# Kernel tuning notes

Hardware: AMD Instinct MI355X
Metric: run time of the kernel (lower is better)

## Reference

```python
import jax, jax.numpy as jnp
import numpy as np

EPS = 1e-5


def _conv(x, w, padding, groups=1):
    return jax.lax.conv_general_dilated(
        x, w, window_strides=(1, 1),
        padding=[(padding, padding), (padding, padding)],
        dimension_numbers=("NCHW", "OIHW", "NCHW"),
        feature_group_count=groups)


def _bn(x, gamma, beta, mean, var):
    # inference-mode BatchNorm2d, params shape [C]
    inv = gamma * jax.lax.rsqrt(var + EPS)
    return x * inv[None, :, None, None] + (beta - mean * inv)[None, :, None, None]


def _adder_dw(x, w):
    # depthwise AdderNet 'conv': out[b, c*R+r, h, w] = -sum_{kh,kw} |x[b,c,h+kh-p,w+kw-p] - w[c,r,kh,kw]|
    # x: [B,C,H,W], w: [C,R,K,K] (groups=C, R outputs per group)
    B, C, H, W = x.shape
    R, K = w.shape[1], w.shape[-1]
    p = K // 2
    xp = jnp.pad(x, ((0, 0), (0, 0), (p, p), (p, p)))
    acc = jnp.zeros((B, C, R, H, W), x.dtype)
    for kh in range(K):          # fixed small 3x3 tap loop
        for kw in range(K):
            shift = xp[:, :, kh:kh + H, kw:kw + W]          # [B,C,H,W]
            tap = w[:, :, kh, kw]                           # [C,R]
            acc = acc + jnp.abs(shift[:, :, None] - tap[None, :, :, None, None])
    return -acc.reshape(B, C * R, H, W)


def setup_inputs() -> dict:
    key = jax.random.key(0)
    ks = jax.random.split(key, 12)
    B, Cin, H, W = 32, 240, 56, 56
    init_c, ratio = 24, 10
    r1 = ratio - 1            # 9 ghost channels per primary channel
    new_c = init_c * r1       # 216
    f32 = jnp.float32
    x = jax.random.normal(ks[0], (B, Cin, H, W), f32)
    w_primary = jax.random.normal(ks[1], (init_c, Cin, 1, 1), f32) * 0.05
    w_dw = jax.random.normal(ks[2], (init_c, 1, 3, 3), f32) * 0.1
    w_add = jax.random.normal(ks[3], (init_c, r1, 3, 3), f32) * 0.1
    def bn(kk, c):
        k1, k2 = jax.random.split(kk)
        return (jnp.ones((c,), f32), jnp.zeros((c,), f32),
                jax.random.normal(k1, (c,), f32) * 0.1,
                jax.random.uniform(k2, (c,), f32, 0.5, 1.5))
    g1, b1, m1, v1 = bn(ks[4], init_c)
    g2, b2, m2, v2 = bn(ks[5], init_c)
    g3, b3, m3, v3 = bn(ks[6], new_c)
    return dict(x=x, w_primary=w_primary, g1=g1, b1=b1, m1=m1, v1=v1,
                w_dw=w_dw, g2=g2, b2=b2, m2=m2, v2=v2,
                w_add=w_add, g3=g3, b3=b3, m3=m3, v3=v3)


def reference(x, w_primary, g1, b1, m1, v1, w_dw, g2, b2, m2, v2,
              w_add, g3, b3, m3, v3):
    oup = 240
    init_c = w_primary.shape[0]
    # primary_conv: 1x1 conv -> BN -> depthwise 3x3 conv -> BN -> Identity (relu slot is Identity)
    x1 = _conv(x, w_primary, padding=0)
    x1 = _bn(x1, g1, b1, m1, v1)
    x1 = _conv(x1, w_dw, padding=1, groups=init_c)
    x1 = _bn(x1, g2, b2, m2, v2)
    # cheap_operation: depthwise Adder2D -> BN -> ReLU
    x2 = _adder_dw(x1, w_add)
    x2 = jax.nn.relu(_bn(x2, g3, b3, m3, v3))
    out = jnp.concatenate([x1, x2], axis=1)
    return out[:, :oup]
```

## Files before the change

kernel.cpp:

```cpp
#include <hip/hip_runtime.h>

#define EPS_ 1e-5f
#define BATCH 32
#define CIN 240
#define H_ 56
#define W_ 56
#define HW 3136
#define C1 24
#define R_ 9
#define C2 216
#define COUT 240

#define WS_WT   0
#define WS_B1   5760
#define WS_WDW  5784
#define WS_B2   6000
#define WS_INV3 6024
#define WS_T3   6240
#define WS_T1   8192
#define WS_T1_FLOATS (8192 + BATCH * C1 * HW)

__global__ __launch_bounds__(256) void prep_kernel(
    const float* __restrict__ wp,
    const float* __restrict__ g1, const float* __restrict__ b1,
    const float* __restrict__ m1, const float* __restrict__ v1,
    const float* __restrict__ wdw,
    const float* __restrict__ g2, const float* __restrict__ b2,
    const float* __restrict__ m2, const float* __restrict__ v2,
    const float* __restrict__ g3, const float* __restrict__ b3,
    const float* __restrict__ m3, const float* __restrict__ v3,
    float* __restrict__ ws) {
  int i = blockIdx.x * 256 + threadIdx.x;
  if (i < 5760) {
    int ci = i / C1, co = i % C1;
    float s = g1[co] / sqrtf(v1[co] + EPS_);
    ws[WS_WT + ci * C1 + co] = wp[co * CIN + ci] * s;
    if (ci == 0) ws[WS_B1 + co] = b1[co] - m1[co] * s;
  } else if (i < 5760 + C2) {
    int j = i - 5760;
    int c = j / 9;
    float s = g2[c] / sqrtf(v2[c] + EPS_);
    ws[WS_WDW + j] = wdw[j] * s;
    if (j % 9 == 0) ws[WS_B2 + c] = b2[c] - m2[c] * s;
  } else if (i < 5976 + C2) {
    int j = i - 5976;
    float s = g3[j] / sqrtf(v3[j] + EPS_);
    ws[WS_INV3 + j] = s;
    ws[WS_T3 + j] = b3[j] - m3[j] * s;
  }
}

__global__ __launch_bounds__(256) void conv1x1_kernel(
    const float* __restrict__ x, const float* __restrict__ wt,
    const float* __restrict__ bias1, float* __restrict__ t1b,
    const int cs, const int coff) {
  __shared__ float smem[6144];
  const int tid  = threadIdx.x;
  const int lane = tid & 63;
  const int kq   = tid >> 6;

  for (int i = tid; i < 5760; i += 256) smem[i] = wt[i];
  __syncthreads();

  const int P   = blockIdx.x * 64 + lane;
  const int b   = P / HW;
  const int hw  = P - b * HW;
  const int ci0 = kq * 60;
  const float* xp    = x + ((size_t)b * CIN + ci0) * HW + hw;
  const float* wbase = smem + ci0 * C1;

  float acc[C1];
#pragma unroll
  for (int i = 0; i < C1; ++i) acc[i] = 0.f;

  float A[6], B[6];
#pragma unroll
  for (int j = 0; j < 6; ++j) A[j] = xp[(size_t)j * HW];
#pragma unroll
  for (int j = 0; j < 6; ++j) B[j] = xp[(size_t)(6 + j) * HW];

  auto consume = [&](const float* buf, int cb) {
#pragma unroll
    for (int j = 0; j < 6; ++j) {
      const float xv = buf[j];
      const float* wr = wbase + (cb + j) * C1;
#pragma unroll
      for (int k = 0; k < 6; ++k) {
        const float4 wq = *(const float4*)(wr + 4 * k);
        acc[4*k+0] = fmaf(wq.x, xv, acc[4*k+0]);
        acc[4*k+1] = fmaf(wq.y, xv, acc[4*k+1]);
        acc[4*k+2] = fmaf(wq.z, xv, acc[4*k+2]);
        acc[4*k+3] = fmaf(wq.w, xv, acc[4*k+3]);
      }
    }
  };

#pragma unroll 1
  for (int g = 0; g < 4; ++g) {
    const int c = 12 * g;
    consume(A, c);
#pragma unroll
    for (int j = 0; j < 6; ++j) A[j] = xp[(size_t)(c + 12 + j) * HW];
    consume(B, c + 6);
#pragma unroll
    for (int j = 0; j < 6; ++j) B[j] = xp[(size_t)(c + 18 + j) * HW];
  }
  consume(A, 48);
  consume(B, 54);
  __syncthreads();

#pragma unroll
  for (int i = 0; i < C1; ++i) smem[(kq * C1 + i) * 64 + lane] = acc[i];
  __syncthreads();

  float* o = t1b + ((size_t)b * cs + coff) * HW + hw;
#pragma unroll
  for (int i = 0; i < 6; ++i) {
    const int co = kq * 6 + i;
    float v = smem[(0 * C1 + co) * 64 + lane]
            + smem[(1 * C1 + co) * 64 + lane]
            + smem[(2 * C1 + co) * 64 + lane]
            + smem[(3 * C1 + co) * 64 + lane]
            + bias1[co];
    o[(size_t)co * HW] = v;
  }
}

__global__ __launch_bounds__(512) void dwadd_kernel(
    const float* __restrict__ t1b, const float* __restrict__ wdwf,
    const float* __restrict__ bias2, const float* __restrict__ wadd,
    const float* __restrict__ inv3, const float* __restrict__ t3,
    float* __restrict__ out) {
  const int c = blockIdx.y, b = blockIdx.z;
  __shared__ __align__(16) float t1s[60 * 56];
  __shared__ __align__(16) float x1s[58 * 56];
  __shared__ float taps[R_][3][4];
  __shared__ float s3[R_], t3s[R_];
  const int tid = threadIdx.x;

  const float* t1 = t1b + ((size_t)b * C1 + c) * HW;
  for (int q = tid; q < 840; q += 512) {
    if (q < 784) {
      const float4 v = *(const float4*)(t1 + q * 4);
      const int rt = q / 14, w0 = (q - rt * 14) * 4;
      *(float4*)&t1s[(rt + 2) * 56 + w0] = v;
    } else {
      const int j = q - 784;
      const int zr = j / 14;
      const int row = (zr < 2) ? zr : zr + 56;
      const int w0 = (j - zr * 14) * 4;
      *(float4*)&t1s[row * 56 + w0] = make_float4(0.f, 0.f, 0.f, 0.f);
    }
  }
  if (tid < 108) {
    int r = tid / 12, kh = (tid / 4) % 3, kw = tid & 3;
    taps[r][kh][kw] = (kw < 3) ? wadd[((c * R_ + r) * 3 + kh) * 3 + kw] : 0.f;
  } else if (tid >= 128 && tid < 128 + R_) {
    int r = tid - 128;
    s3[r]  = inv3[c * R_ + r];
    t3s[r] = t3[c * R_ + r];
  }
  float wk[9];
#pragma unroll
  for (int k = 0; k < 9; ++k) wk[k] = wdwf[c * 9 + k];
  const float bb = bias2[c];
  __syncthreads();

  float* xout = out + ((size_t)b * COUT + c) * HW;
  for (int q = tid; q < 812; q += 512) {
    const int r  = q / 14;
    const int w0 = (q - r * 14) * 4;
    const int gr = r - 1;
    float4 v = {bb, bb, bb, bb};
#pragma unroll
    for (int kh = 0; kh < 3; ++kh) {
      const float* rp = &t1s[(r + kh) * 56];
      const float  l  = (w0 > 0) ? rp[w0 - 1] : 0.f;
      const float4 m  = *(const float4*)(rp + w0);
      const float  rt = (w0 < 52) ? rp[w0 + 4] : 0.f;
      const float t0 = wk[kh * 3 + 0], t1w = wk[kh * 3 + 1], t2 = wk[kh * 3 + 2];
      v.x = fmaf(l,   t0, v.x); v.x = fmaf(m.x, t1w, v.x); v.x = fmaf(m.y, t2, v.x);
      v.y = fmaf(m.x, t0, v.y); v.y = fmaf(m.y, t1w, v.y); v.y = fmaf(m.z, t2, v.y);
      v.z = fmaf(m.y, t0, v.z); v.z = fmaf(m.z, t1w, v.z); v.z = fmaf(m.w, t2, v.z);
      v.w = fmaf(m.z, t0, v.w); v.w = fmaf(m.w, t1w, v.w); v.w = fmaf(rt,  t2, v.w);
    }
    float4 xv = v;
    if (gr < 0 || gr >= H_) { xv.x = 0.f; xv.y = 0.f; xv.z = 0.f; xv.w = 0.f; }
    *(float4*)&x1s[r * 56 + w0] = xv;
    if (gr >= 0 && gr < H_)
      *(float4*)(xout + gr * W_ + w0) = v;
  }
  __syncthreads();

  float* obase = out + ((size_t)b * COUT + C1 + c * R_) * HW;
  for (int q = tid; q < 784; q += 512) {
    const int gr = q / 14;
    const int w0 = (q - gr * 14) * 4;
    float xr[3][6];
#pragma unroll
    for (int kh = 0; kh < 3; ++kh) {
      const float* rp = &x1s[(gr + kh) * 56];
      xr[kh][0] = (w0 > 0) ? rp[w0 - 1] : 0.f;
      const float4 m = *(const float4*)(rp + w0);
      xr[kh][1] = m.x; xr[kh][2] = m.y; xr[kh][3] = m.z; xr[kh][4] = m.w;
      xr[kh][5] = (w0 < 52) ? rp[w0 + 4] : 0.f;
    }
    float* ob = obase + gr * W_ + w0;
#pragma unroll
    for (int rr = 0; rr < R_; ++rr) {
      float a0 = 0.f, a1 = 0.f, a2 = 0.f, a3 = 0.f;
#pragma unroll
      for (int kh = 0; kh < 3; ++kh) {
#pragma unroll
        for (int kw = 0; kw < 3; ++kw) {
          const float t = taps[rr][kh][kw];
          a0 += fabsf(xr[kh][kw + 0] - t);
          a1 += fabsf(xr[kh][kw + 1] - t);
          a2 += fabsf(xr[kh][kw + 2] - t);
          a3 += fabsf(xr[kh][kw + 3] - t);
        }
      }
      const float s = s3[rr], tb = t3s[rr];
      float4 v;
      v.x = fmaxf(fmaf(-s, a0, tb), 0.f);
      v.y = fmaxf(fmaf(-s, a1, tb), 0.f);
      v.z = fmaxf(fmaf(-s, a2, tb), 0.f);
      v.w = fmaxf(fmaf(-s, a3, tb), 0.f);
      *(float4*)(ob + (size_t)rr * HW) = v;
    }
  }
}


__global__ __launch_bounds__(256) void dw_kernel(
    const float* __restrict__ outr, const float* __restrict__ wdwf,
    const float* __restrict__ bias2, float* __restrict__ out) {
  const int c = blockIdx.y, b = blockIdx.z;
  const int q = blockIdx.x * 256 + threadIdx.x;
  if (q >= 784) return;
  const int h  = q / 14;
  const int w0 = (q - h * 14) * 4;
  const float* in = outr + ((size_t)b * COUT + C1 + c) * HW;

  float wk[9];
#pragma unroll
  for (int k = 0; k < 9; ++k) wk[k] = wdwf[c * 9 + k];
  const float bb = bias2[c];

  float xr[3][6];
#pragma unroll
  for (int kh = 0; kh < 3; ++kh) {
    const int hh = h + kh - 1;
    const bool rok = (hh >= 0) & (hh < H_);
    const float* rp = in + hh * W_;
    xr[kh][0] = (rok && w0 > 0) ? rp[w0 - 1] : 0.f;
    if (rok) {
      const float4 m = *(const float4*)(rp + w0);
      xr[kh][1] = m.x; xr[kh][2] = m.y; xr[kh][3] = m.z; xr[kh][4] = m.w;
    } else {
      xr[kh][1] = 0.f; xr[kh][2] = 0.f; xr[kh][3] = 0.f; xr[kh][4] = 0.f;
    }
    xr[kh][5] = (rok && w0 < W_ - 4) ? rp[w0 + 4] : 0.f;
  }

  float4 v = {bb, bb, bb, bb};
#pragma unroll
  for (int kh = 0; kh < 3; ++kh) {
#pragma unroll
    for (int kw = 0; kw < 3; ++kw) {
      const float t = wk[kh * 3 + kw];
      v.x = fmaf(xr[kh][kw + 0], t, v.x);
      v.y = fmaf(xr[kh][kw + 1], t, v.y);
      v.z = fmaf(xr[kh][kw + 2], t, v.z);
      v.w = fmaf(xr[kh][kw + 3], t, v.w);
    }
  }
  *(float4*)(out + ((size_t)b * COUT + c) * HW + h * W_ + w0) = v;
}

__global__ __launch_bounds__(256) void adder_kernel(
    const float* __restrict__ outr, const float* __restrict__ wadd,
    const float* __restrict__ inv3, const float* __restrict__ t3,
    float* __restrict__ out) {
  const int c = blockIdx.y, b = blockIdx.z;
  __shared__ float taps[R_][3][4];
  __shared__ float s3[R_], t3s[R_];
  const int tid = threadIdx.x;
  if (tid < 108) {
    int r = tid / 12, kh = (tid / 4) % 3, kw = tid & 3;
    taps[r][kh][kw] = (kw < 3) ? wadd[((c * R_ + r) * 3 + kh) * 3 + kw] : 0.f;
  } else if (tid >= 128 && tid < 128 + R_) {
    int r = tid - 128;
    s3[r]  = inv3[c * R_ + r];
    t3s[r] = t3[c * R_ + r];
  }
  __syncthreads();

  const int q = blockIdx.x * 256 + tid;
  if (q >= 784) return;
  const int h  = q / 14;
  const int w0 = (q - h * 14) * 4;
  const float* in = outr + ((size_t)b * COUT + C1 + c) * HW;

  float xr[3][6];
#pragma unroll
  for (int kh = 0; kh < 3; ++kh) {
    const int hh = h + kh - 1;
    const bool rok = (hh >= 0) & (hh < H_);
    const float* rp = in + hh * W_;
    xr[kh][0] = (rok && w0 > 0) ? rp[w0 - 1] : 0.f;
    if (rok) {
      const float4 m = *(const float4*)(rp + w0);
      xr[kh][1] = m.x; xr[kh][2] = m.y; xr[kh][3] = m.z; xr[kh][4] = m.w;
    } else {
      xr[kh][1] = 0.f; xr[kh][2] = 0.f; xr[kh][3] = 0.f; xr[kh][4] = 0.f;
    }
    xr[kh][5] = (rok && w0 < W_ - 4) ? rp[w0 + 4] : 0.f;
  }

#pragma unroll
  for (int r = 0; r < R_; ++r) {
    float a0 = 0.f, a1 = 0.f, a2 = 0.f, a3 = 0.f;
#pragma unroll
    for (int kh = 0; kh < 3; ++kh) {
#pragma unroll
      for (int kw = 0; kw < 3; ++kw) {
        const float t = taps[r][kh][kw];
        a0 += fabsf(xr[kh][kw + 0] - t);
        a1 += fabsf(xr[kh][kw + 1] - t);
        a2 += fabsf(xr[kh][kw + 2] - t);
        a3 += fabsf(xr[kh][kw + 3] - t);
      }
    }
    const float s = s3[r], bb = t3s[r];
    float4 v;
    v.x = fmaxf(fmaf(-s, a0, bb), 0.f);
    v.y = fmaxf(fmaf(-s, a1, bb), 0.f);
    v.z = fmaxf(fmaf(-s, a2, bb), 0.f);
    v.w = fmaxf(fmaf(-s, a3, bb), 0.f);
    *(float4*)(out + ((size_t)b * COUT + C1 + c * R_ + r) * HW + h * W_ + w0) = v;
  }
}

extern "C" void kernel_launch(void* const* d_in, const int* in_sizes, int n_in,
                              void* d_out, int out_size, void* d_ws, size_t ws_size,
                              hipStream_t stream) {
  const float* x    = (const float*)d_in[0];
  const float* wp   = (const float*)d_in[1];
  const float* g1   = (const float*)d_in[2];
  const float* b1   = (const float*)d_in[3];
  const float* m1   = (const float*)d_in[4];
  const float* v1   = (const float*)d_in[5];
  const float* wdw  = (const float*)d_in[6];
  const float* g2   = (const float*)d_in[7];
  const float* b2   = (const float*)d_in[8];
  const float* m2   = (const float*)d_in[9];
  const float* v2   = (const float*)d_in[10];
  const float* wadd = (const float*)d_in[11];
  const float* g3   = (const float*)d_in[12];
  const float* b3   = (const float*)d_in[13];
  const float* m3   = (const float*)d_in[14];
  const float* v3   = (const float*)d_in[15];

  float* ws  = (float*)d_ws;
  float* out = (float*)d_out;

  const bool fused = ws_size >= (size_t)WS_T1_FLOATS * sizeof(float);
  float* t1b;
  int cs, coff;
  if (fused) { t1b = ws + WS_T1; cs = C1;   coff = 0; }
  else       { t1b = out;        cs = COUT; coff = C1; }

  prep_kernel<<<25, 256, 0, stream>>>(wp, g1, b1, m1, v1, wdw, g2, b2, m2, v2,
                                      g3, b3, m3, v3, ws);

  conv1x1_kernel<<<1568, 256, 0, stream>>>(x, ws + WS_WT, ws + WS_B1,
                                           t1b, cs, coff);

  if (fused) {
    dwadd_kernel<<<dim3(1, C1, BATCH), 512, 0, stream>>>(
        t1b, ws + WS_WDW, ws + WS_B2, wadd, ws + WS_INV3, ws + WS_T3, out);
  } else {
    dw_kernel<<<dim3(4, C1, BATCH), 256, 0, stream>>>(out, ws + WS_WDW,
                                                      ws + WS_B2, out);
    adder_kernel<<<dim3(4, C1, BATCH), 256, 0, stream>>>(out, wadd,
                                                         ws + WS_INV3,
                                                         ws + WS_T3, out);
  }
}
```

Baseline: 217.8 us.

## Fold BN parameter prep into consumer kernels and compute two pixels per thread in conv1x1

```diff
diff --git a/kernel.cpp b/kernel.cpp
--- a/kernel.cpp
+++ b/kernel.cpp
@@ -11,86 +11,59 @@
 #define C2 216
 #define COUT 240
 
-#define WS_WT   0
-#define WS_B1   5760
-#define WS_WDW  5784
-#define WS_B2   6000
-#define WS_INV3 6024
-#define WS_T3   6240
-#define WS_T1   8192
-#define WS_T1_FLOATS (8192 + BATCH * C1 * HW)
-
-__global__ __launch_bounds__(256) void prep_kernel(
-    const float* __restrict__ wp,
+#define WS_T1   0
+#define WS_T1_FLOATS (BATCH * C1 * HW)
+
+__global__ __launch_bounds__(256, 3) void conv1x1_kernel(
+    const float* __restrict__ x, const float* __restrict__ wp,
     const float* __restrict__ g1, const float* __restrict__ b1,
     const float* __restrict__ m1, const float* __restrict__ v1,
-    const float* __restrict__ wdw,
-    const float* __restrict__ g2, const float* __restrict__ b2,
-    const float* __restrict__ m2, const float* __restrict__ v2,
-    const float* __restrict__ g3, const float* __restrict__ b3,
-    const float* __restrict__ m3, const float* __restrict__ v3,
-    float* __restrict__ ws) {
-  int i = blockIdx.x * 256 + threadIdx.x;
-  if (i < 5760) {
-    int ci = i / C1, co = i % C1;
-    float s = g1[co] / sqrtf(v1[co] + EPS_);
-    ws[WS_WT + ci * C1 + co] = wp[co * CIN + ci] * s;
-    if (ci == 0) ws[WS_B1 + co] = b1[co] - m1[co] * s;
-  } else if (i < 5760 + C2) {
-    int j = i - 5760;
-    int c = j / 9;
-    float s = g2[c] / sqrtf(v2[c] + EPS_);
-    ws[WS_WDW + j] = wdw[j] * s;
-    if (j % 9 == 0) ws[WS_B2 + c] = b2[c] - m2[c] * s;
-  } else if (i < 5976 + C2) {
-    int j = i - 5976;
-    float s = g3[j] / sqrtf(v3[j] + EPS_);
-    ws[WS_INV3 + j] = s;
-    ws[WS_T3 + j] = b3[j] - m3[j] * s;
-  }
-}
-
-__global__ __launch_bounds__(256) void conv1x1_kernel(
-    const float* __restrict__ x, const float* __restrict__ wt,
-    const float* __restrict__ bias1, float* __restrict__ t1b,
-    const int cs, const int coff) {
-  __shared__ float smem[6144];
+    float* __restrict__ t1b, const int cs, const int coff) {
+  __shared__ float smem[12288];
   const int tid  = threadIdx.x;
   const int lane = tid & 63;
   const int kq   = tid >> 6;
 
-  for (int i = tid; i < 5760; i += 256) smem[i] = wt[i];
-  __syncthreads();
-
-  const int P   = blockIdx.x * 64 + lane;
+  for (int i = tid; i < 5760; i += 256) {
+    const int ci = i / C1, co = i - ci * C1;
+    const float s = g1[co] / sqrtf(v1[co] + EPS_);
+    smem[i] = wp[co * CIN + ci] * s;
+  }
+  __syncthreads();
+
+  const int P   = blockIdx.x * 128 + lane * 2;
   const int b   = P / HW;
   const int hw  = P - b * HW;
   const int ci0 = kq * 60;
   const float* xp    = x + ((size_t)b * CIN + ci0) * HW + hw;
   const float* wbase = smem + ci0 * C1;
 
-  float acc[C1];
-#pragma unroll
-  for (int i = 0; i < C1; ++i) acc[i] = 0.f;
-
-  float A[6], B[6];
-#pragma unroll
-  for (int j = 0; j < 6; ++j) A[j] = xp[(size_t)j * HW];
-#pragma unroll
-  for (int j = 0; j < 6; ++j) B[j] = xp[(size_t)(6 + j) * HW];
-
-  auto consume = [&](const float* buf, int cb) {
+  float acc[C1][2];
+#pragma unroll
+  for (int i = 0; i < C1; ++i) { acc[i][0] = 0.f; acc[i][1] = 0.f; }
+
+  float2 A[6], B[6];
+#pragma unroll
+  for (int j = 0; j < 6; ++j) A[j] = *(const float2*)(xp + (size_t)j * HW);
+#pragma unroll
+  for (int j = 0; j < 6; ++j) B[j] = *(const float2*)(xp + (size_t)(6 + j) * HW);
+
+  auto consume = [&](const float2* buf, int cb) {
 #pragma unroll
     for (int j = 0; j < 6; ++j) {
-      const float xv = buf[j];
+      const float2 xv = buf[j];
       const float* wr = wbase + (cb + j) * C1;
 #pragma unroll
       for (int k = 0; k < 6; ++k) {
         const float4 wq = *(const float4*)(wr + 4 * k);
-        acc[4*k+0] = fmaf(wq.x, xv, acc[4*k+0]);
-        acc[4*k+1] = fmaf(wq.y, xv, acc[4*k+1]);
-        acc[4*k+2] = fmaf(wq.z, xv, acc[4*k+2]);
-        acc[4*k+3] = fmaf(wq.w, xv, acc[4*k+3]);
+        acc[4*k+0][0] = fmaf(wq.x, xv.x, acc[4*k+0][0]);
+        acc[4*k+0][1] = fmaf(wq.x, xv.y, acc[4*k+0][1]);
+        acc[4*k+1][0] = fmaf(wq.y, xv.x, acc[4*k+1][0]);
+        acc[4*k+1][1] = fmaf(wq.y, xv.y, acc[4*k+1][1]);
+        acc[4*k+2][0] = fmaf(wq.z, xv.x, acc[4*k+2][0]);
+        acc[4*k+2][1] = fmaf(wq.z, xv.y, acc[4*k+2][1]);
+        acc[4*k+3][0] = fmaf(wq.w, xv.x, acc[4*k+3][0]);
+        acc[4*k+3][1] = fmaf(wq.w, xv.y, acc[4*k+3][1]);
       }
     }
   };
@@ -100,36 +73,45 @@
     const int c = 12 * g;
     consume(A, c);
 #pragma unroll
-    for (int j = 0; j < 6; ++j) A[j] = xp[(size_t)(c + 12 + j) * HW];
+    for (int j = 0; j < 6; ++j) A[j] = *(const float2*)(xp + (size_t)(c + 12 + j) * HW);
     consume(B, c + 6);
 #pragma unroll
-    for (int j = 0; j < 6; ++j) B[j] = xp[(size_t)(c + 18 + j) * HW];
+    for (int j = 0; j < 6; ++j) B[j] = *(const float2*)(xp + (size_t)(c + 18 + j) * HW);
   }
   consume(A, 48);
   consume(B, 54);
   __syncthreads();
 
 #pragma unroll
-  for (int i = 0; i < C1; ++i) smem[(kq * C1 + i) * 64 + lane] = acc[i];
+  for (int i = 0; i < C1; ++i)
+    *(float2*)&smem[(kq * C1 + i) * 128 + 2 * lane] = make_float2(acc[i][0], acc[i][1]);
   __syncthreads();
 
   float* o = t1b + ((size_t)b * cs + coff) * HW + hw;
 #pragma unroll
   for (int i = 0; i < 6; ++i) {
     const int co = kq * 6 + i;
-    float v = smem[(0 * C1 + co) * 64 + lane]
-            + smem[(1 * C1 + co) * 64 + lane]
-            + smem[(2 * C1 + co) * 64 + lane]
-            + smem[(3 * C1 + co) * 64 + lane]
-            + bias1[co];
-    o[(size_t)co * HW] = v;
+    const float2 p0 = *(const float2*)&smem[(0 * C1 + co) * 128 + 2 * lane];
+    const float2 p1 = *(const float2*)&smem[(1 * C1 + co) * 128 + 2 * lane];
+    const float2 p2 = *(const float2*)&smem[(2 * C1 + co) * 128 + 2 * lane];
+    const float2 p3 = *(const float2*)&smem[(3 * C1 + co) * 128 + 2 * lane];
+    const float sc  = g1[co] / sqrtf(v1[co] + EPS_);
+    const float bsv = b1[co] - m1[co] * sc;
+    float2 v;
+    v.x = p0.x + p1.x + p2.x + p3.x + bsv;
+    v.y = p0.y + p1.y + p2.y + p3.y + bsv;
+    *(float2*)(o + (size_t)co * HW) = v;
   }
 }
 
 __global__ __launch_bounds__(512) void dwadd_kernel(
-    const float* __restrict__ t1b, const float* __restrict__ wdwf,
-    const float* __restrict__ bias2, const float* __restrict__ wadd,
-    const float* __restrict__ inv3, const float* __restrict__ t3,
+    const float* __restrict__ t1b,
+    const float* __restrict__ wdw,
+    const float* __restrict__ g2, const float* __restrict__ b2,
+    const float* __restrict__ m2, const float* __restrict__ v2,
+    const float* __restrict__ wadd,
+    const float* __restrict__ g3, const float* __restrict__ b3,
+    const float* __restrict__ m3, const float* __restrict__ v3,
     float* __restrict__ out) {
   const int c = blockIdx.y, b = blockIdx.z;
   __shared__ __align__(16) float t1s[60 * 56];
@@ -157,13 +139,16 @@
     taps[r][kh][kw] = (kw < 3) ? wadd[((c * R_ + r) * 3 + kh) * 3 + kw] : 0.f;
   } else if (tid >= 128 && tid < 128 + R_) {
     int r = tid - 128;
-    s3[r]  = inv3[c * R_ + r];
-    t3s[r] = t3[c * R_ + r];
-  }
+    const int j = c * R_ + r;
+    const float s = g3[j] / sqrtf(v3[j] + EPS_);
+    s3[r]  = s;
+    t3s[r] = b3[j] - m3[j] * s;
+  }
+  const float s2 = g2[c] / sqrtf(v2[c] + EPS_);
   float wk[9];
 #pragma unroll
-  for (int k = 0; k < 9; ++k) wk[k] = wdwf[c * 9 + k];
-  const float bb = bias2[c];
+  for (int k = 0; k < 9; ++k) wk[k] = wdw[c * 9 + k] * s2;
+  const float bb = b2[c] - m2[c] * s2;
   __syncthreads();
 
   float* xout = out + ((size_t)b * COUT + c) * HW;
@@ -233,8 +218,10 @@
 
 
 __global__ __launch_bounds__(256) void dw_kernel(
-    const float* __restrict__ outr, const float* __restrict__ wdwf,
-    const float* __restrict__ bias2, float* __restrict__ out) {
+    const float* __restrict__ outr, const float* __restrict__ wdw,
+    const float* __restrict__ g2, const float* __restrict__ b2,
+    const float* __restrict__ m2, const float* __restrict__ v2,
+    float* __restrict__ out) {
   const int c = blockIdx.y, b = blockIdx.z;
   const int q = blockIdx.x * 256 + threadIdx.x;
   if (q >= 784) return;
@@ -242,10 +229,11 @@
   const int w0 = (q - h * 14) * 4;
   const float* in = outr + ((size_t)b * COUT + C1 + c) * HW;
 
+  const float s2 = g2[c] / sqrtf(v2[c] + EPS_);
   float wk[9];
 #pragma unroll
-  for (int k = 0; k < 9; ++k) wk[k] = wdwf[c * 9 + k];
-  const float bb = bias2[c];
+  for (int k = 0; k < 9; ++k) wk[k] = wdw[c * 9 + k] * s2;
+  const float bb = b2[c] - m2[c] * s2;
 
   float xr[3][6];
 #pragma unroll
@@ -280,7 +268,8 @@
 
 __global__ __launch_bounds__(256) void adder_kernel(
     const float* __restrict__ outr, const float* __restrict__ wadd,
-    const float* __restrict__ inv3, const float* __restrict__ t3,
+    const float* __restrict__ g3, const float* __restrict__ b3,
+    const float* __restrict__ m3, const float* __restrict__ v3,
     float* __restrict__ out) {
   const int c = blockIdx.y, b = blockIdx.z;
   __shared__ float taps[R_][3][4];
@@ -291,8 +280,10 @@
     taps[r][kh][kw] = (kw < 3) ? wadd[((c * R_ + r) * 3 + kh) * 3 + kw] : 0.f;
   } else if (tid >= 128 && tid < 128 + R_) {
     int r = tid - 128;
-    s3[r]  = inv3[c * R_ + r];
-    t3s[r] = t3[c * R_ + r];
+    const int j = c * R_ + r;
+    const float s = g3[j] / sqrtf(v3[j] + EPS_);
+    s3[r]  = s;
+    t3s[r] = b3[j] - m3[j] * s;
   }
   __syncthreads();
 
@@ -371,20 +362,16 @@
   if (fused) { t1b = ws + WS_T1; cs = C1;   coff = 0; }
   else       { t1b = out;        cs = COUT; coff = C1; }
 
-  prep_kernel<<<25, 256, 0, stream>>>(wp, g1, b1, m1, v1, wdw, g2, b2, m2, v2,
-                                      g3, b3, m3, v3, ws);
-
-  conv1x1_kernel<<<1568, 256, 0, stream>>>(x, ws + WS_WT, ws + WS_B1,
-                                           t1b, cs, coff);
+  conv1x1_kernel<<<784, 256, 0, stream>>>(x, wp, g1, b1, m1, v1,
+                                          t1b, cs, coff);
 
   if (fused) {
     dwadd_kernel<<<dim3(1, C1, BATCH), 512, 0, stream>>>(
-        t1b, ws + WS_WDW, ws + WS_B2, wadd, ws + WS_INV3, ws + WS_T3, out);
+        t1b, wdw, g2, b2, m2, v2, wadd, g3, b3, m3, v3, out);
   } else {
-    dw_kernel<<<dim3(4, C1, BATCH), 256, 0, stream>>>(out, ws + WS_WDW,
-                                                      ws + WS_B2, out);
+    dw_kernel<<<dim3(4, C1, BATCH), 256, 0, stream>>>(out, wdw,
+                                                      g2, b2, m2, v2, out);
     adder_kernel<<<dim3(4, C1, BATCH), 256, 0, stream>>>(out, wadd,
-                                                         ws + WS_INV3,
-                                                         ws + WS_T3, out);
-  }
-}
+                                                         g3, b3, m3, v3, out);
+  }
+}
```

Result: slower. 321.1 us (+47.4%).
